# Kernel optimization log

Measured on AMD Instinct MI355X. Metric: run time of the kernel, lower is better.

## Reference

```python
import jax, jax.numpy as jnp
import numpy as np

B, N, T, C = 4, 4096, 16, 64
E = 32768
K = 3
EPS = 1e-5


def setup_inputs() -> dict:
    key = jax.random.key(0)
    ks = jax.random.split(key, 12)
    s = 0.05
    return {
        "x": jax.random.normal(ks[0], (B, N, T, C), dtype=jnp.float32),
        "edge_src": jax.random.randint(ks[1], (E,), 0, N, dtype=jnp.int32),
        "edge_dst": jax.random.randint(ks[2], (E,), 0, N, dtype=jnp.int32),
        "edge_weight": jax.random.uniform(ks[3], (E,), dtype=jnp.float32),
        "W1": jax.random.normal(ks[4], (2 * C, C, K), dtype=jnp.float32) * s,
        "b1": jax.random.normal(ks[5], (2 * C,), dtype=jnp.float32) * s,
        "Wg": jax.random.normal(ks[6], (C, C), dtype=jnp.float32) * s,
        "bg": jax.random.normal(ks[7], (C,), dtype=jnp.float32) * s,
        "W2": jax.random.normal(ks[8], (2 * C, C, K), dtype=jnp.float32) * s,
        "b2": jax.random.normal(ks[9], (2 * C,), dtype=jnp.float32) * s,
        "gamma": jnp.ones((C,), dtype=jnp.float32),
        "beta": jnp.zeros((C,), dtype=jnp.float32),
    }


def temporal_glu(x, W, b):
    # x: (B, N, T, Cin) -> (B, N, T, Cout); 'same' conv along T with GLU gating
    Bb, Nn, Tt, Cc = x.shape
    co = W.shape[0] // 2
    h = x.reshape(Bb * Nn, Tt, Cc).transpose(0, 2, 1)  # (BN, C, T)
    pad = (K - 1) // 2
    h = jax.lax.conv_general_dilated(
        h, W, window_strides=(1,), padding=[(pad, pad)],
        dimension_numbers=("NCH", "OIH", "NCH")) + b[None, :, None]
    value, gate = h[:, :co, :], h[:, co:, :]
    h = value * jax.nn.sigmoid(gate)
    return h.transpose(0, 2, 1).reshape(Bb, Nn, Tt, co)


def spatial_gcn(x, Wg, bg, edge_src, edge_dst, edge_weight):
    # linear projection then sparse aggregation: out[i] = sum_j A[i,j] y[j]
    y = jnp.einsum("bntc,dc->bntd", x, Wg) + bg
    Bb, Nn, Tt, Cc = y.shape
    y2 = y.transpose(1, 0, 2, 3).reshape(Nn, Bb * Tt * Cc)  # (N, BTC)
    msg = edge_weight[:, None] * y2[edge_dst]               # (E, BTC)
    agg = jax.ops.segment_sum(msg, edge_src, num_segments=Nn)
    return agg.reshape(Nn, Bb, Tt, Cc).transpose(1, 0, 2, 3)


def reference(x, edge_src, edge_dst, edge_weight, W1, b1, Wg, bg, W2, b2, gamma, beta):
    residual = x  # c_in == c_out -> Identity residual; T preserved by padding
    out = jax.nn.relu(temporal_glu(x, W1, b1))
    out = jax.nn.relu(spatial_gcn(out, Wg, bg, edge_src, edge_dst, edge_weight))
    out = temporal_glu(out, W2, b2)
    out = out + residual
    # BatchNorm2d over (B, N, T) per channel C (training-mode batch stats)
    mean = jnp.mean(out, axis=(0, 1, 2))
    var = jnp.var(out, axis=(0, 1, 2))
    out = (out - mean) * jax.lax.rsqrt(var + EPS) * gamma + beta
    # dropout is identity in eval/deterministic mode
    return jax.nn.relu(out)
```

## Files before the change

### kernel.cpp

```cpp
#include <hip/hip_runtime.h>

#define NB 4
#define NN 4096
#define NT 16
#define NC 64
#define NE 32768
#define XR 72
#define MPB 2

typedef unsigned int uint;
typedef unsigned char uchar;
typedef unsigned short ushort;

typedef short bf16x8 __attribute__((ext_vector_type(8)));
typedef float f32x4 __attribute__((ext_vector_type(4)));

union ABu { uint2 u2[2]; bf16x8 v; };

__device__ inline ushort f2b(float f) {
  union { float f; uint u; } v; v.f = f;
  uint r = v.u + 0x7FFF + ((v.u >> 16) & 1);
  return (ushort)(r >> 16);
}
__device__ inline float blo(uint u) { union { uint i; float f; } v; v.i = u << 16; return v.f; }
__device__ inline float bhi(uint u) { union { uint i; float f; } v; v.i = u & 0xffff0000u; return v.f; }
__device__ inline uchar f2fp8(float f) {
  int w = __builtin_amdgcn_cvt_pk_fp8_f32(f, f, 0, false);
  return (uchar)(w & 0xff);
}

__global__ void k_prep(const float* __restrict__ W1, const float* __restrict__ W2,
                       const float* __restrict__ Wg,
                       ushort* __restrict__ Bp1, ushort* __restrict__ Bp2,
                       ushort* __restrict__ Wgp, int* __restrict__ count) {
  int i = blockIdx.x * blockDim.x + threadIdx.x;
  if (i < 24576) {
    int j = i & 7, l = (i >> 3) & 63, nt = (i >> 9) & 7, s = i >> 12;
    int kap = 32 * s + 4 * (l >> 4) + (j & 3) + 16 * (j >> 2);
    int c = kap & 63, kk = kap >> 6, o = nt * 16 + (l & 15);
    Bp1[i] = f2b(W1[o * 192 + c * 3 + kk]);
    Bp2[i] = f2b(W2[o * 192 + c * 3 + kk]);
  } else if (i < 28672) {
    int i2 = i - 24576;
    int j = i2 & 7, l = (i2 >> 3) & 63, nt2 = (i2 >> 9) & 3, s2 = i2 >> 11;
    int kap = 32 * s2 + 4 * (l >> 4) + (j & 3) + 16 * (j >> 2);
    int d = nt2 * 16 + (l & 15);
    Wgp[i2] = f2b(Wg[d * 64 + kap]);
  } else {
    count[i - 28672] = 0;
  }
}

__global__ void k_count(const int* __restrict__ src, int* __restrict__ count) {
  int e = blockIdx.x * blockDim.x + threadIdx.x;
  if (e < NE) atomicAdd(&count[src[e]], 1);
}

__global__ void k_scan(const int* __restrict__ count, int* __restrict__ offsets,
                       int* __restrict__ cursor) {
  __shared__ int part[256];
  int tid = threadIdx.x;
  int base = tid * 16;
  int s = 0;
  for (int i = 0; i < 16; ++i) s += count[base + i];
  part[tid] = s;
  __syncthreads();
  if (tid == 0) {
    int r = 0;
    for (int i = 0; i < 256; ++i) { int t = part[i]; part[i] = r; r += t; }
    offsets[NN] = r;
  }
  __syncthreads();
  int r = part[tid];
  for (int i = 0; i < 16; ++i) {
    offsets[base + i] = r;
    cursor[base + i] = r;
    r += count[base + i];
  }
}

__global__ void k_place(const int* __restrict__ src, const int* __restrict__ dst,
                        const float* __restrict__ ew, int* __restrict__ cursor,
                        int* __restrict__ dsts, float* __restrict__ wsrt) {
  int e = blockIdx.x * blockDim.x + threadIdx.x;
  if (e < NE) {
    int p = atomicAdd(&cursor[src[e]], 1);
    dsts[p] = dst[e];
    wsrt[p] = ew[e];
  }
}

__global__ __launch_bounds__(256, 3) void k_glu1lin(
    const float* __restrict__ x, const ushort* __restrict__ Bp1,
    const float* __restrict__ b1, const ushort* __restrict__ Wgp,
    const float* __restrict__ bg, uchar* __restrict__ y) {
  __shared__ ushort As[MPB * 4 * 18 * XR + 64 * 68];
  ushort* hs = As + MPB * 4 * 18 * XR;
  int tid = threadIdx.x;
  int n0 = blockIdx.x * MPB;
  int w = tid >> 6, l = tid & 63, m = l & 15, g4 = l >> 4;

  bf16x8 bc[6][2];
  #pragma unroll
  for (int s = 0; s < 6; ++s) {
    bc[s][0] = *(const bf16x8*)&Bp1[((s * 8 + w) * 64 + l) * 8];
    bc[s][1] = *(const bf16x8*)&Bp1[((s * 8 + w + 4) * 64 + l) * 8];
  }
  bf16x8 wg2[2];
  #pragma unroll
  for (int s2 = 0; s2 < 2; ++s2)
    wg2[s2] = *(const bf16x8*)&Wgp[((s2 * 4 + w) * 64 + l) * 8];

  {
    int nd = tid >> 7, rem = tid & 127;
    int b = rem >> 5, tp = ((rem >> 4) & 1) ? 17 : 0, c4 = (rem & 15) * 4;
    *(uint2*)&As[((nd * 4 + b) * 18 + tp) * XR + c4] = make_uint2(0, 0);
  }
  const float4* x4 = (const float4*)x;
  #pragma unroll
  for (int q = 0; q < 8; ++q) {
    int f4 = q * 256 + tid;
    int nd = f4 >> 10, rem = f4 & 1023;
    int b = rem >> 8, r = rem & 255, tau = r >> 4, c4i = r & 15;
    float4 v = x4[((b * NN + n0 + nd) * 16 + tau) * 16 + c4i];
    uint2 p;
    p.x = (uint)f2b(v.x) | ((uint)f2b(v.y) << 16);
    p.y = (uint)f2b(v.z) | ((uint)f2b(v.w) << 16);
    *(uint2*)&As[((nd * 4 + b) * 18 + tau + 1) * XR + c4i * 4] = p;
  }
  __syncthreads();

  float bv = b1[w * 16 + m], bgate = b1[64 + w * 16 + m];
  float bgl = bg[w * 16 + m];

  #pragma unroll
  for (int nd = 0; nd < MPB; ++nd) {
    int nd4 = nd * 4;
    f32x4 acc[4][2];
    #pragma unroll
    for (int rt = 0; rt < 4; ++rt) {
      acc[rt][0] = (f32x4){bv, bv, bv, bv};
      acc[rt][1] = (f32x4){bgate, bgate, bgate, bgate};
    }
    #pragma unroll
    for (int s = 0; s < 6; ++s) {
      const int kk = s >> 1, sp = s & 1;
      int col = 32 * sp + 4 * g4;
      #pragma unroll
      for (int rt = 0; rt < 4; ++rt) {
        int r0 = ((nd4 + rt) * 18 + m + kk) * XR + col;
        ABu a;
        a.u2[0] = *(const uint2*)&As[r0];
        a.u2[1] = *(const uint2*)&As[r0 + 16];
        acc[rt][0] = __builtin_amdgcn_mfma_f32_16x16x32_bf16(a.v, bc[s][0], acc[rt][0], 0, 0, 0);
        acc[rt][1] = __builtin_amdgcn_mfma_f32_16x16x32_bf16(a.v, bc[s][1], acc[rt][1], 0, 0, 0);
      }
    }
    #pragma unroll
    for (int rt = 0; rt < 4; ++rt)
      #pragma unroll
      for (int i = 0; i < 4; ++i) {
        float v = acc[rt][0][i], gt = acc[rt][1][i];
        float h = fmaxf(v / (1.f + __expf(-gt)), 0.f);
        hs[(rt * 16 + 4 * g4 + i) * 68 + w * 16 + m] = f2b(h);
      }
    __syncthreads();

    f32x4 acc2[4];
    #pragma unroll
    for (int rt = 0; rt < 4; ++rt) acc2[rt] = (f32x4){bgl, bgl, bgl, bgl};
    #pragma unroll
    for (int s2 = 0; s2 < 2; ++s2) {
      #pragma unroll
      for (int rt = 0; rt < 4; ++rt) {
        int rb = (rt * 16 + m) * 68 + 32 * s2 + 4 * g4;
        ABu a;
        a.u2[0] = *(const uint2*)&hs[rb];
        a.u2[1] = *(const uint2*)&hs[rb + 16];
        acc2[rt] = __builtin_amdgcn_mfma_f32_16x16x32_bf16(a.v, wg2[s2], acc2[rt], 0, 0, 0);
      }
    }
    uchar* yb = y + ((size_t)(n0 + nd) * NB) * 1024;
    #pragma unroll
    for (int rt = 0; rt < 4; ++rt)
      #pragma unroll
      for (int i = 0; i < 4; ++i) {
        int t = 4 * g4 + i;
        yb[rt * 1024 + t * 64 + w * 16 + m] = f2fp8(acc2[rt][i]);
      }
    __syncthreads();
  }
}

__global__ __launch_bounds__(256) void k_gather(
    const uchar* __restrict__ y, const int* __restrict__ offsets,
    const int* __restrict__ dsts, const float* __restrict__ wsrt,
    ushort* __restrict__ agg) {
  int tid = threadIdx.x;
  int blk = blockIdx.x;
  int n = blk >> 1, s = blk & 1;
  int base = s * 2048 + tid * 8;
  int e0 = offsets[n], e1 = offsets[n + 1];

  float a0 = 0, a1 = 0, a2 = 0, a3 = 0, a4 = 0, a5 = 0, a6 = 0, a7 = 0;
  int e = e0;
  for (; e + 2 <= e1; e += 2) {
    int d0 = dsts[e], d1 = dsts[e + 1];
    float w0 = wsrt[e], w1 = wsrt[e + 1];
    uint2 v0 = *(const uint2*)(y + (size_t)d0 * 4096 + base);
    uint2 v1 = *(const uint2*)(y + (size_t)d1 * 4096 + base);
    a0 += w0 * __builtin_amdgcn_cvt_f32_fp8(v0.x, 0);
    a1 += w0 * __builtin_amdgcn_cvt_f32_fp8(v0.x, 1);
    a2 += w0 * __builtin_amdgcn_cvt_f32_fp8(v0.x, 2);
    a3 += w0 * __builtin_amdgcn_cvt_f32_fp8(v0.x, 3);
    a4 += w0 * __builtin_amdgcn_cvt_f32_fp8(v0.y, 0);
    a5 += w0 * __builtin_amdgcn_cvt_f32_fp8(v0.y, 1);
    a6 += w0 * __builtin_amdgcn_cvt_f32_fp8(v0.y, 2);
    a7 += w0 * __builtin_amdgcn_cvt_f32_fp8(v0.y, 3);
    a0 += w1 * __builtin_amdgcn_cvt_f32_fp8(v1.x, 0);
    a1 += w1 * __builtin_amdgcn_cvt_f32_fp8(v1.x, 1);
    a2 += w1 * __builtin_amdgcn_cvt_f32_fp8(v1.x, 2);
    a3 += w1 * __builtin_amdgcn_cvt_f32_fp8(v1.x, 3);
    a4 += w1 * __builtin_amdgcn_cvt_f32_fp8(v1.y, 0);
    a5 += w1 * __builtin_amdgcn_cvt_f32_fp8(v1.y, 1);
    a6 += w1 * __builtin_amdgcn_cvt_f32_fp8(v1.y, 2);
    a7 += w1 * __builtin_amdgcn_cvt_f32_fp8(v1.y, 3);
  }
  if (e < e1) {
    int d0 = dsts[e];
    float w0 = wsrt[e];
    uint2 v0 = *(const uint2*)(y + (size_t)d0 * 4096 + base);
    a0 += w0 * __builtin_amdgcn_cvt_f32_fp8(v0.x, 0);
    a1 += w0 * __builtin_amdgcn_cvt_f32_fp8(v0.x, 1);
    a2 += w0 * __builtin_amdgcn_cvt_f32_fp8(v0.x, 2);
    a3 += w0 * __builtin_amdgcn_cvt_f32_fp8(v0.x, 3);
    a4 += w0 * __builtin_amdgcn_cvt_f32_fp8(v0.y, 0);
    a5 += w0 * __builtin_amdgcn_cvt_f32_fp8(v0.y, 1);
    a6 += w0 * __builtin_amdgcn_cvt_f32_fp8(v0.y, 2);
    a7 += w0 * __builtin_amdgcn_cvt_f32_fp8(v0.y, 3);
  }
  uint4 o;
  o.x = (uint)f2b(fmaxf(a0, 0.f)) | ((uint)f2b(fmaxf(a1, 0.f)) << 16);
  o.y = (uint)f2b(fmaxf(a2, 0.f)) | ((uint)f2b(fmaxf(a3, 0.f)) << 16);
  o.z = (uint)f2b(fmaxf(a4, 0.f)) | ((uint)f2b(fmaxf(a5, 0.f)) << 16);
  o.w = (uint)f2b(fmaxf(a6, 0.f)) | ((uint)f2b(fmaxf(a7, 0.f)) << 16);
  *(uint4*)(agg + (size_t)n * 4096 + base) = o;
}

__global__ __launch_bounds__(256, 3) void k_glu2(
    const ushort* __restrict__ agg, const float* __restrict__ x,
    const ushort* __restrict__ Bp2, const float* __restrict__ b2,
    float* __restrict__ out, float* __restrict__ partials) {
  __shared__ ushort As[MPB * 4 * 18 * XR];
  __shared__ float red[512];
  int tid = threadIdx.x;
  int n0 = blockIdx.x * MPB;
  int w = tid >> 6, l = tid & 63, m = l & 15, g4 = l >> 4;

  bf16x8 bc[6][2];
  #pragma unroll
  for (int s = 0; s < 6; ++s) {
    bc[s][0] = *(const bf16x8*)&Bp2[((s * 8 + w) * 64 + l) * 8];
    bc[s][1] = *(const bf16x8*)&Bp2[((s * 8 + w + 4) * 64 + l) * 8];
  }

  {
    int nd = tid >> 7, rem = tid & 127;
    int b = rem >> 5, tp = ((rem >> 4) & 1) ? 17 : 0, c4 = (rem & 15) * 4;
    *(uint2*)&As[((nd * 4 + b) * 18 + tp) * XR + c4] = make_uint2(0, 0);
  }
  const uint4* ag4 = (const uint4*)agg;
  #pragma unroll
  for (int q = 0; q < 4; ++q) {
    int u = q * 256 + tid;
    int nd = u >> 9, rem = u & 511;
    int b = rem >> 7, r = rem & 127, tau = r >> 3, c0 = (r & 7) * 8;
    uint4 v = ag4[(size_t)(n0 + nd) * 512 + rem];
    *(uint4*)&As[((nd * 4 + b) * 18 + tau + 1) * XR + c0] = v;
  }
  __syncthreads();

  float bv = b2[w * 16 + m], bgate = b2[64 + w * 16 + m];
  float p1 = 0.f, p2 = 0.f;

  #pragma unroll
  for (int nd = 0; nd < MPB; ++nd) {
    int n = n0 + nd, nd4 = nd * 4;
    float xr[4][4];
    #pragma unroll
    for (int rt = 0; rt < 4; ++rt) {
      const float* xb = x + ((size_t)rt * NN + n) * 1024 + w * 16 + m;
      #pragma unroll
      for (int i = 0; i < 4; ++i)
        xr[rt][i] = xb[(4 * g4 + i) * 64];
    }
    f32x4 acc[4][2];
    #pragma unroll
    for (int rt = 0; rt < 4; ++rt) {
      acc[rt][0] = (f32x4){bv, bv, bv, bv};
      acc[rt][1] = (f32x4){bgate, bgate, bgate, bgate};
    }
    #pragma unroll
    for (int s = 0; s < 6; ++s) {
      const int kk = s >> 1, sp = s & 1;
      int col = 32 * sp + 4 * g4;
      #pragma unroll
      for (int rt = 0; rt < 4; ++rt) {
        int r0 = ((nd4 + rt) * 18 + m + kk) * XR + col;
        ABu a;
        a.u2[0] = *(const uint2*)&As[r0];
        a.u2[1] = *(const uint2*)&As[r0 + 16];
        acc[rt][0] = __builtin_amdgcn_mfma_f32_16x16x32_bf16(a.v, bc[s][0], acc[rt][0], 0, 0, 0);
        acc[rt][1] = __builtin_amdgcn_mfma_f32_16x16x32_bf16(a.v, bc[s][1], acc[rt][1], 0, 0, 0);
      }
    }
    #pragma unroll
    for (int rt = 0; rt < 4; ++rt)
      #pragma unroll
      for (int i = 0; i < 4; ++i) {
        float v = acc[rt][0][i], gt = acc[rt][1][i];
        float h = v / (1.f + __expf(-gt));
        int t = 4 * g4 + i;
        float res = h + xr[rt][i];
        out[((rt * NN + n) * 16 + t) * 64 + w * 16 + m] = res;
        p1 += res;
        p2 += res * res;
      }
  }
  red[(w * 16 + m) * 4 + g4] = p1;
  red[256 + (w * 16 + m) * 4 + g4] = p2;
  __syncthreads();
  if (tid < 64) {
    float s = red[tid * 4] + red[tid * 4 + 1] + red[tid * 4 + 2] + red[tid * 4 + 3];
    partials[tid * (NN / MPB) + blockIdx.x] = s;
  } else if (tid < 128) {
    int c = tid - 64;
    float s = red[256 + c * 4] + red[256 + c * 4 + 1] + red[256 + c * 4 + 2] + red[256 + c * 4 + 3];
    partials[(64 + c) * (NN / MPB) + blockIdx.x] = s;
  }
}

__global__ __launch_bounds__(256) void k_reduce(const float* __restrict__ partials,
                                                float* __restrict__ chan) {
  __shared__ float sm[256];
  int r = blockIdx.x, tid = threadIdx.x;
  const float* p = partials + (size_t)r * (NN / MPB);
  float s = 0.f;
  for (int i = tid; i < NN / MPB; i += 256) s += p[i];
  sm[tid] = s;
  __syncthreads();
  for (int w = 128; w >= 1; w >>= 1) {
    if (tid < w) sm[tid] += sm[tid + w];
    __syncthreads();
  }
  if (tid == 0) chan[r] = sm[0];
}

__global__ __launch_bounds__(256) void k_norm(
    float* __restrict__ out, const float* __restrict__ chan,
    const float* __restrict__ gamma, const float* __restrict__ beta) {
  __shared__ float sc[64], sh[64];
  int tid = threadIdx.x;
  if (tid < 64) {
    const float inv = 1.f / (float)(NB * NN * NT);
    float mean = chan[tid] * inv;
    float var = chan[64 + tid] * inv - mean * mean;
    float s = rsqrtf(var + 1e-5f) * gamma[tid];
    sc[tid] = s;
    sh[tid] = beta[tid] - mean * s;
  }
  __syncthreads();
  float4* o4 = (float4*)out;
  const int total = NB * NN * NT * 16;
  for (int i = blockIdx.x * blockDim.x + threadIdx.x; i < total;
       i += gridDim.x * blockDim.x) {
    float4 v = o4[i];
    int c = (i * 4) & 63;
    v.x = fmaxf(v.x * sc[c + 0] + sh[c + 0], 0.f);
    v.y = fmaxf(v.y * sc[c + 1] + sh[c + 1], 0.f);
    v.z = fmaxf(v.z * sc[c + 2] + sh[c + 2], 0.f);
    v.w = fmaxf(v.w * sc[c + 3] + sh[c + 3], 0.f);
    o4[i] = v;
  }
}


extern "C" void kernel_launch(void* const* d_in, const int* in_sizes, int n_in,
                              void* d_out, int out_size, void* d_ws, size_t ws_size,
                              hipStream_t stream) {
  const float* x    = (const float*)d_in[0];
  const int* esrc   = (const int*)d_in[1];
  const int* edst   = (const int*)d_in[2];
  const float* ew   = (const float*)d_in[3];
  const float* W1   = (const float*)d_in[4];
  const float* b1   = (const float*)d_in[5];
  const float* Wg   = (const float*)d_in[6];
  const float* bg   = (const float*)d_in[7];
  const float* W2   = (const float*)d_in[8];
  const float* b2   = (const float*)d_in[9];
  const float* gamma = (const float*)d_in[10];
  const float* beta  = (const float*)d_in[11];
  float* out = (float*)d_out;

  uchar* y8      = (uchar*)d_ws;
  ushort* agg_bf = (ushort*)(y8 + 16777216);
  ushort* Bp1    = agg_bf + 16777216;
  ushort* Bp2    = Bp1 + 24576;
  ushort* Wgp    = Bp2 + 24576;
  float* chan    = (float*)(Wgp + 4096);
  int* count   = (int*)(chan + 128);
  int* offsets = count + 4096;
  int* cursor  = offsets + 4097;
  int* dsts    = cursor + 4096;
  float* wsrt  = (float*)(dsts + NE);
  float* partials = (float*)y8;

  hipLaunchKernelGGL(k_prep, dim3(128), dim3(256), 0, stream, W1, W2, Wg, Bp1, Bp2, Wgp, count);
  hipLaunchKernelGGL(k_count, dim3(128), dim3(256), 0, stream, esrc, count);
  hipLaunchKernelGGL(k_scan, dim3(1), dim3(256), 0, stream, count, offsets, cursor);
  hipLaunchKernelGGL(k_place, dim3(128), dim3(256), 0, stream, esrc, edst, ew, cursor, dsts, wsrt);
  hipLaunchKernelGGL(k_glu1lin, dim3(NN / MPB), dim3(256), 0, stream,
                     x, Bp1, b1, Wgp, bg, y8);
  hipLaunchKernelGGL(k_gather, dim3(NN * 2), dim3(256), 0, stream,
                     y8, offsets, dsts, wsrt, agg_bf);
  hipLaunchKernelGGL(k_glu2, dim3(NN / MPB), dim3(256), 0, stream,
                     agg_bf, x, Bp2, b2, out, partials);
  hipLaunchKernelGGL(k_reduce, dim3(128), dim3(256), 0, stream, partials, chan);
  hipLaunchKernelGGL(k_norm, dim3(2048), dim3(256), 0, stream,
                     out, chan, gamma, beta);
}
```

Measured before the change: 124.9 us.

## Fuse sparse gather into second GLU kernel and store pre-norm output as bf16

Removes the separate gather kernel: each k_glu2 block now aggregates neighbour rows from the fp8 y buffer directly into shared memory, so the bf16 agg intermediate is never written to or read back from global memory. The pre-normalisation output is also stored as bf16 in workspace, and k_norm reads it and writes fp32, halving that intermediate's traffic. The trade-off is less parallelism for the gather (2048 blocks doing 2 nodes each instead of 8192 blocks), possible register pressure under launch_bounds(256,3), and extra rounding of the residual sum before normalisation.

```diff
diff --git a/kernel.cpp b/kernel.cpp
--- a/kernel.cpp
+++ b/kernel.cpp
@@ -27,6 +27,12 @@
 __device__ inline uchar f2fp8(float f) {
   int w = __builtin_amdgcn_cvt_pk_fp8_f32(f, f, 0, false);
   return (uchar)(w & 0xff);
+}
+__device__ inline void fp8x4(uint u, float* o) {
+  o[0] = __builtin_amdgcn_cvt_f32_fp8(u, 0);
+  o[1] = __builtin_amdgcn_cvt_f32_fp8(u, 1);
+  o[2] = __builtin_amdgcn_cvt_f32_fp8(u, 2);
+  o[3] = __builtin_amdgcn_cvt_f32_fp8(u, 3);
 }
 
 __global__ void k_prep(const float* __restrict__ W1, const float* __restrict__ W2,
@@ -192,65 +198,12 @@
   }
 }
 
-__global__ __launch_bounds__(256) void k_gather(
-    const uchar* __restrict__ y, const int* __restrict__ offsets,
-    const int* __restrict__ dsts, const float* __restrict__ wsrt,
-    ushort* __restrict__ agg) {
-  int tid = threadIdx.x;
-  int blk = blockIdx.x;
-  int n = blk >> 1, s = blk & 1;
-  int base = s * 2048 + tid * 8;
-  int e0 = offsets[n], e1 = offsets[n + 1];
-
-  float a0 = 0, a1 = 0, a2 = 0, a3 = 0, a4 = 0, a5 = 0, a6 = 0, a7 = 0;
-  int e = e0;
-  for (; e + 2 <= e1; e += 2) {
-    int d0 = dsts[e], d1 = dsts[e + 1];
-    float w0 = wsrt[e], w1 = wsrt[e + 1];
-    uint2 v0 = *(const uint2*)(y + (size_t)d0 * 4096 + base);
-    uint2 v1 = *(const uint2*)(y + (size_t)d1 * 4096 + base);
-    a0 += w0 * __builtin_amdgcn_cvt_f32_fp8(v0.x, 0);
-    a1 += w0 * __builtin_amdgcn_cvt_f32_fp8(v0.x, 1);
-    a2 += w0 * __builtin_amdgcn_cvt_f32_fp8(v0.x, 2);
-    a3 += w0 * __builtin_amdgcn_cvt_f32_fp8(v0.x, 3);
-    a4 += w0 * __builtin_amdgcn_cvt_f32_fp8(v0.y, 0);
-    a5 += w0 * __builtin_amdgcn_cvt_f32_fp8(v0.y, 1);
-    a6 += w0 * __builtin_amdgcn_cvt_f32_fp8(v0.y, 2);
-    a7 += w0 * __builtin_amdgcn_cvt_f32_fp8(v0.y, 3);
-    a0 += w1 * __builtin_amdgcn_cvt_f32_fp8(v1.x, 0);
-    a1 += w1 * __builtin_amdgcn_cvt_f32_fp8(v1.x, 1);
-    a2 += w1 * __builtin_amdgcn_cvt_f32_fp8(v1.x, 2);
-    a3 += w1 * __builtin_amdgcn_cvt_f32_fp8(v1.x, 3);
-    a4 += w1 * __builtin_amdgcn_cvt_f32_fp8(v1.y, 0);
-    a5 += w1 * __builtin_amdgcn_cvt_f32_fp8(v1.y, 1);
-    a6 += w1 * __builtin_amdgcn_cvt_f32_fp8(v1.y, 2);
-    a7 += w1 * __builtin_amdgcn_cvt_f32_fp8(v1.y, 3);
-  }
-  if (e < e1) {
-    int d0 = dsts[e];
-    float w0 = wsrt[e];
-    uint2 v0 = *(const uint2*)(y + (size_t)d0 * 4096 + base);
-    a0 += w0 * __builtin_amdgcn_cvt_f32_fp8(v0.x, 0);
-    a1 += w0 * __builtin_amdgcn_cvt_f32_fp8(v0.x, 1);
-    a2 += w0 * __builtin_amdgcn_cvt_f32_fp8(v0.x, 2);
-    a3 += w0 * __builtin_amdgcn_cvt_f32_fp8(v0.x, 3);
-    a4 += w0 * __builtin_amdgcn_cvt_f32_fp8(v0.y, 0);
-    a5 += w0 * __builtin_amdgcn_cvt_f32_fp8(v0.y, 1);
-    a6 += w0 * __builtin_amdgcn_cvt_f32_fp8(v0.y, 2);
-    a7 += w0 * __builtin_amdgcn_cvt_f32_fp8(v0.y, 3);
-  }
-  uint4 o;
-  o.x = (uint)f2b(fmaxf(a0, 0.f)) | ((uint)f2b(fmaxf(a1, 0.f)) << 16);
-  o.y = (uint)f2b(fmaxf(a2, 0.f)) | ((uint)f2b(fmaxf(a3, 0.f)) << 16);
-  o.z = (uint)f2b(fmaxf(a4, 0.f)) | ((uint)f2b(fmaxf(a5, 0.f)) << 16);
-  o.w = (uint)f2b(fmaxf(a6, 0.f)) | ((uint)f2b(fmaxf(a7, 0.f)) << 16);
-  *(uint4*)(agg + (size_t)n * 4096 + base) = o;
-}
-
 __global__ __launch_bounds__(256, 3) void k_glu2(
-    const ushort* __restrict__ agg, const float* __restrict__ x,
+    const uchar* __restrict__ y8, const float* __restrict__ x,
     const ushort* __restrict__ Bp2, const float* __restrict__ b2,
-    float* __restrict__ out, float* __restrict__ partials) {
+    const int* __restrict__ offsets, const int* __restrict__ dsts,
+    const float* __restrict__ wsrt,
+    ushort* __restrict__ outb, float* __restrict__ partials) {
   __shared__ ushort As[MPB * 4 * 18 * XR];
   __shared__ float red[512];
   int tid = threadIdx.x;
@@ -269,14 +222,46 @@
     int b = rem >> 5, tp = ((rem >> 4) & 1) ? 17 : 0, c4 = (rem & 15) * 4;
     *(uint2*)&As[((nd * 4 + b) * 18 + tp) * XR + c4] = make_uint2(0, 0);
   }
-  const uint4* ag4 = (const uint4*)agg;
-  #pragma unroll
-  for (int q = 0; q < 4; ++q) {
-    int u = q * 256 + tid;
-    int nd = u >> 9, rem = u & 511;
-    int b = rem >> 7, r = rem & 127, tau = r >> 3, c0 = (r & 7) * 8;
-    uint4 v = ag4[(size_t)(n0 + nd) * 512 + rem];
-    *(uint4*)&As[((nd * 4 + b) * 18 + tau + 1) * XR + c0] = v;
+
+  #pragma unroll
+  for (int nd = 0; nd < MPB; ++nd) {
+    int n = n0 + nd;
+    int e0 = offsets[n], e1 = offsets[n + 1];
+    float ga[16];
+    #pragma unroll
+    for (int j = 0; j < 16; ++j) ga[j] = 0.f;
+    const uchar* ybase = y8 + tid * 16;
+    int e = e0;
+    for (; e + 2 <= e1; e += 2) {
+      int d0 = dsts[e], d1 = dsts[e + 1];
+      float w0 = wsrt[e], w1 = wsrt[e + 1];
+      uint4 v0 = *(const uint4*)(ybase + (size_t)d0 * 4096);
+      uint4 v1 = *(const uint4*)(ybase + (size_t)d1 * 4096);
+      float f0[16], f1[16];
+      fp8x4(v0.x, f0); fp8x4(v0.y, f0 + 4); fp8x4(v0.z, f0 + 8); fp8x4(v0.w, f0 + 12);
+      fp8x4(v1.x, f1); fp8x4(v1.y, f1 + 4); fp8x4(v1.z, f1 + 8); fp8x4(v1.w, f1 + 12);
+      #pragma unroll
+      for (int j = 0; j < 16; ++j)
+        ga[j] += w0 * f0[j] + w1 * f1[j];
+    }
+    if (e < e1) {
+      int d0 = dsts[e];
+      float w0 = wsrt[e];
+      uint4 v0 = *(const uint4*)(ybase + (size_t)d0 * 4096);
+      float f0[16];
+      fp8x4(v0.x, f0); fp8x4(v0.y, f0 + 4); fp8x4(v0.z, f0 + 8); fp8x4(v0.w, f0 + 12);
+      #pragma unroll
+      for (int j = 0; j < 16; ++j)
+        ga[j] += w0 * f0[j];
+    }
+    int b = tid >> 6, t = (tid >> 2) & 15, c0 = (tid & 3) * 16;
+    uint pk[8];
+    #pragma unroll
+    for (int j = 0; j < 8; ++j)
+      pk[j] = (uint)f2b(fmaxf(ga[2 * j], 0.f)) | ((uint)f2b(fmaxf(ga[2 * j + 1], 0.f)) << 16);
+    ushort* dstp = &As[((nd * 4 + b) * 18 + t + 1) * XR + c0];
+    *(uint4*)dstp = make_uint4(pk[0], pk[1], pk[2], pk[3]);
+    *(uint4*)(dstp + 8) = make_uint4(pk[4], pk[5], pk[6], pk[7]);
   }
   __syncthreads();
 
@@ -322,7 +307,7 @@
         float h = v / (1.f + __expf(-gt));
         int t = 4 * g4 + i;
         float res = h + xr[rt][i];
-        out[((rt * NN + n) * 16 + t) * 64 + w * 16 + m] = res;
+        outb[((rt * NN + n) * 16 + t) * 64 + w * 16 + m] = f2b(res);
         p1 += res;
         p2 += res * res;
       }
@@ -357,8 +342,9 @@
 }
 
 __global__ __launch_bounds__(256) void k_norm(
-    float* __restrict__ out, const float* __restrict__ chan,
-    const float* __restrict__ gamma, const float* __restrict__ beta) {
+    const ushort* __restrict__ outb, float* __restrict__ out,
+    const float* __restrict__ chan, const float* __restrict__ gamma,
+    const float* __restrict__ beta) {
   __shared__ float sc[64], sh[64];
   int tid = threadIdx.x;
   if (tid < 64) {
@@ -370,17 +356,23 @@
     sh[tid] = beta[tid] - mean * s;
   }
   __syncthreads();
-  float4* o4 = (float4*)out;
-  const int total = NB * NN * NT * 16;
+  const uint4* i4 = (const uint4*)outb;
+  const int total = NB * NN * NT * 8;
   for (int i = blockIdx.x * blockDim.x + threadIdx.x; i < total;
        i += gridDim.x * blockDim.x) {
-    float4 v = o4[i];
-    int c = (i * 4) & 63;
-    v.x = fmaxf(v.x * sc[c + 0] + sh[c + 0], 0.f);
-    v.y = fmaxf(v.y * sc[c + 1] + sh[c + 1], 0.f);
-    v.z = fmaxf(v.z * sc[c + 2] + sh[c + 2], 0.f);
-    v.w = fmaxf(v.w * sc[c + 3] + sh[c + 3], 0.f);
-    o4[i] = v;
+    uint4 v = i4[i];
+    int c0 = (i & 7) * 8;
+    float4 o0, o1;
+    o0.x = fmaxf(blo(v.x) * sc[c0 + 0] + sh[c0 + 0], 0.f);
+    o0.y = fmaxf(bhi(v.x) * sc[c0 + 1] + sh[c0 + 1], 0.f);
+    o0.z = fmaxf(blo(v.y) * sc[c0 + 2] + sh[c0 + 2], 0.f);
+    o0.w = fmaxf(bhi(v.y) * sc[c0 + 3] + sh[c0 + 3], 0.f);
+    o1.x = fmaxf(blo(v.z) * sc[c0 + 4] + sh[c0 + 4], 0.f);
+    o1.y = fmaxf(bhi(v.z) * sc[c0 + 5] + sh[c0 + 5], 0.f);
+    o1.z = fmaxf(blo(v.w) * sc[c0 + 6] + sh[c0 + 6], 0.f);
+    o1.w = fmaxf(bhi(v.w) * sc[c0 + 7] + sh[c0 + 7], 0.f);
+    ((float4*)out)[i * 2] = o0;
+    ((float4*)out)[i * 2 + 1] = o1;
   }
 }
 
@@ -403,8 +395,8 @@
   float* out = (float*)d_out;
 
   uchar* y8      = (uchar*)d_ws;
-  ushort* agg_bf = (ushort*)(y8 + 16777216);
-  ushort* Bp1    = agg_bf + 16777216;
+  ushort* outb   = (ushort*)(y8 + 16777216);
+  ushort* Bp1    = outb + 16777216;
   ushort* Bp2    = Bp1 + 24576;
   ushort* Wgp    = Bp2 + 24576;
   float* chan    = (float*)(Wgp + 4096);
@@ -413,7 +405,7 @@
   int* cursor  = offsets + 4097;
   int* dsts    = cursor + 4096;
   float* wsrt  = (float*)(dsts + NE);
-  float* partials = (float*)y8;
+  float* partials = wsrt + NE;
 
   hipLaunchKernelGGL(k_prep, dim3(128), dim3(256), 0, stream, W1, W2, Wg, Bp1, Bp2, Wgp, count);
   hipLaunchKernelGGL(k_count, dim3(128), dim3(256), 0, stream, esrc, count);
@@ -421,11 +413,9 @@
   hipLaunchKernelGGL(k_place, dim3(128), dim3(256), 0, stream, esrc, edst, ew, cursor, dsts, wsrt);
   hipLaunchKernelGGL(k_glu1lin, dim3(NN / MPB), dim3(256), 0, stream,
                      x, Bp1, b1, Wgp, bg, y8);
-  hipLaunchKernelGGL(k_gather, dim3(NN * 2), dim3(256), 0, stream,
-                     y8, offsets, dsts, wsrt, agg_bf);
   hipLaunchKernelGGL(k_glu2, dim3(NN / MPB), dim3(256), 0, stream,
-                     agg_bf, x, Bp2, b2, out, partials);
+                     y8, x, Bp2, b2, offsets, dsts, wsrt, outb, partials);
   hipLaunchKernelGGL(k_reduce, dim3(128), dim3(256), 0, stream, partials, chan);
   hipLaunchKernelGGL(k_norm, dim3(2048), dim3(256), 0, stream,
-                     out, chan, gamma, beta);
-}
+                     outb, out, chan, gamma, beta);
+}
```

New measurement: 109.6 us. -12.2%, faster.
